# Kernel optimization log

Measured on AMD Instinct MI355X. Metric: run time of the kernel, lower is better.

Reference implementation:

```python
import jax, jax.numpy as jnp
import numpy as np

HEADS = 8
EMBED = 768
FFN = 4 * EMBED
LN_EPS = 1e-5


def _layernorm(x, g, b):
    m = jnp.mean(x, axis=-1, keepdims=True)
    v = jnp.var(x, axis=-1, keepdims=True)
    return (x - m) * jax.lax.rsqrt(v + LN_EPS) * g + b


def _attention(xn, ctx, Wq, Wkv, Wo, bo, mask):
    # xn: [B, N, C], ctx: [B, M, C], mask: [B, 1, N, M] bool (True = keep)
    B, N, C = xn.shape
    d = C // HEADS
    q = (xn @ Wq).reshape(B, N, HEADS, d).transpose(0, 2, 1, 3)          # b h i d
    k, v = jnp.split(ctx @ Wkv, 2, axis=-1)
    k = k.reshape(B, -1, HEADS, d).transpose(0, 2, 1, 3)                 # b h j d
    v = v.reshape(B, -1, HEADS, d).transpose(0, 2, 1, 3)
    sim = jnp.einsum('bhid,bhjd->bhij', q, k) * (d ** -0.5)
    sim = jnp.where(mask, sim, -jnp.finfo(sim.dtype).max)
    attn = jax.nn.softmax(sim, axis=-1)
    out = jnp.einsum('bhij,bhjd->bhid', attn, v)
    out = out.transpose(0, 2, 1, 3).reshape(B, N, C)
    return out @ Wo + bo


def _block(x, c, effect_lengths, us_rate,
           Wq1, Wkv1, Wo1, bo1, Wq2, Wkv2, Wo2, bo2,
           g1, b1, g2, b2, g4, b4, gc, bc, Wf1, bf1, Wf2, bf2):
    B, L, C = x.shape
    S = c.shape[1]
    el = effect_lengths * us_rate                                        # [B]
    i = jnp.arange(L)
    j_self = jnp.arange(L)
    j_cross = jnp.arange(S)
    # ragged per-sample masks, broadcast over heads: [B, 1, L, L] / [B, 1, L, S]
    mask1 = ((i[None, :, None] < el[:, None, None]) &
             (j_self[None, None, :] < el[:, None, None]))[:, None]
    mask2 = ((i[None, :, None] < el[:, None, None]) &
             (j_cross[None, None, :] < effect_lengths[:, None, None]))[:, None]

    xn = _layernorm(x, g1, b1)
    x = x + _attention(xn, xn, Wq1, Wkv1, Wo1, bo1, mask1)
    xn = _layernorm(x, g2, b2)
    cn = _layernorm(c, gc, bc)
    x = x + _attention(xn, cn, Wq2, Wkv2, Wo2, bo2, mask2)
    xn = _layernorm(x, g4, b4)
    x = x + (jax.nn.gelu(xn @ Wf1 + bf1, approximate=False) @ Wf2 + bf2)
    return x


def setup_inputs() -> dict:
    key = jax.random.key(0)
    ks = jax.random.split(key, 20)
    B, S, US = 8, 512, 2
    L = S * US
    s = 0.02
    inp = {
        'x': jax.random.normal(ks[0], (B, L, EMBED), jnp.float32),
        'c': jax.random.normal(ks[1], (B, S, EMBED), jnp.float32),
        'effect_lengths': jax.random.randint(ks[2], (B,), 1, S + 1),
        'us_rate': US,
        'Wq1': jax.random.normal(ks[3], (EMBED, EMBED), jnp.float32) * s,
        'Wkv1': jax.random.normal(ks[4], (EMBED, 2 * EMBED), jnp.float32) * s,
        'Wo1': jax.random.normal(ks[5], (EMBED, EMBED), jnp.float32) * s,
        'bo1': jnp.zeros((EMBED,), jnp.float32),
        'Wq2': jax.random.normal(ks[6], (EMBED, EMBED), jnp.float32) * s,
        'Wkv2': jax.random.normal(ks[7], (EMBED, 2 * EMBED), jnp.float32) * s,
        'Wo2': jax.random.normal(ks[8], (EMBED, EMBED), jnp.float32) * s,
        'bo2': jnp.zeros((EMBED,), jnp.float32),
        'g1': jnp.ones((EMBED,), jnp.float32), 'b1': jnp.zeros((EMBED,), jnp.float32),
        'g2': jnp.ones((EMBED,), jnp.float32), 'b2': jnp.zeros((EMBED,), jnp.float32),
        'g4': jnp.ones((EMBED,), jnp.float32), 'b4': jnp.zeros((EMBED,), jnp.float32),
        'gc': jnp.ones((EMBED,), jnp.float32), 'bc': jnp.zeros((EMBED,), jnp.float32),
        'Wf1': jax.random.normal(ks[9], (EMBED, FFN), jnp.float32) * s,
        'bf1': jnp.zeros((FFN,), jnp.float32),
        'Wf2': jax.random.normal(ks[10], (FFN, EMBED), jnp.float32) * s,
        'bf2': jnp.zeros((EMBED,), jnp.float32),
    }
    return inp


def reference(x, c, effect_lengths, us_rate,
              Wq1, Wkv1, Wo1, bo1, Wq2, Wkv2, Wo2, bo2,
              g1, b1, g2, b2, g4, b4, gc, bc, Wf1, bf1, Wf2, bf2):
    return _block(x, c, effect_lengths, us_rate,
                  Wq1, Wkv1, Wo1, bo1, Wq2, Wkv2, Wo2, bo2,
                  g1, b1, g2, b2, g4, b4, gc, bc, Wf1, bf1, Wf2, bf2)
```

## Files before the change

kernel.cpp:

```cpp
#include <hip/hip_runtime.h>
#include <math.h>

#define EMBED 768
#define HEADS 8
#define HDIM  96
#define NEG_MASK (-1.0e30f)

typedef unsigned short u16;
typedef unsigned int   u32;

typedef __attribute__((ext_vector_type(4))) float f32x4;
typedef __attribute__((ext_vector_type(8))) short short8;

__device__ __forceinline__ float bf2f(u16 u) {
    return __uint_as_float(((u32)u) << 16);
}
__device__ __forceinline__ u16 f2bf(float f) {
    u32 x = __float_as_uint(f);
    u32 r = (x + 0x7fffu + ((x >> 16) & 1u)) >> 16;
    return (u16)r;
}
__device__ __forceinline__ void unpack2(u32 w, float& lo, float& hi) {
    lo = __uint_as_float(w << 16);
    hi = __uint_as_float(w & 0xffff0000u);
}
__device__ __forceinline__ float wget(const void* p, size_t i, int wf) {
    return wf ? ((const float*)p)[i] : bf2f(((const u16*)p)[i]);
}
__device__ __forceinline__ int bswz(int r, int g) {
    return ((g ^ (r & 3) ^ ((r >> 2) & 3) ^ ((r >> 4) & 3)) << 3);
}

__global__ __launch_bounds__(64) void detect_kernel(const u16* __restrict__ x,
                                                    const int* __restrict__ el,
                                                    const int* __restrict__ usp,
                                                    int* __restrict__ blk) {
    int lane = threadIdx.x;
    int cnt = 0;
    for (int i = lane; i < 4096; i += 64) {
        u32 e = (x[i] >> 7) & 0xFFu;
        if (e >= 0xC0u) cnt++;
    }
#pragma unroll
    for (int off = 32; off > 0; off >>= 1) cnt += __shfl_xor(cnt, off, 64);
    if (lane == 0) {
        blk[0] = (cnt > 32) ? 1 : 0;
        bool i64 = (el[1] == 0) && (el[3] == 0) && (el[5] == 0) && (el[7] == 0);
        for (int b = 0; b < 8; b++) blk[1 + b] = i64 ? el[2 * b] : el[b];
        blk[9] = usp[0];
    }
}

__global__ void wire_to_f32(const void* __restrict__ in, size_t ioff,
                            float* __restrict__ out, int n,
                            const int* __restrict__ blk) {
    int i = blockIdx.x * blockDim.x + threadIdx.x;
    int wf = blk[0];
    if (i < n) out[i] = wget(in, ioff + (size_t)i, wf);
}
__global__ void wire_copy(const void* __restrict__ in, void* __restrict__ out,
                          int n, const int* __restrict__ blk) {
    int i = blockIdx.x * blockDim.x + threadIdx.x;
    int wf = blk[0];
    if (i < n) {
        if (wf) ((float*)out)[i] = ((const float*)in)[i];
        else    ((u16*)out)[i]   = ((const u16*)in)[i];
    }
}
__global__ void f32_to_out(const float* __restrict__ in, void* __restrict__ out,
                           size_t ooff, int n, const int* __restrict__ blk) {
    int i = blockIdx.x * blockDim.x + threadIdx.x;
    int wf = blk[0];
    if (i < n) {
        if (wf) ((float*)out)[ooff + i] = in[i];
        else    ((u16*)out)[ooff + i]   = f2bf(in[i]);
    }
}

__global__ __launch_bounds__(256) void wtrans_kernel(const void* __restrict__ W, size_t woff,
                                                     int ldw, int K,
                                                     u16* __restrict__ WT,
                                                     const int* __restrict__ blk) {
    __shared__ u16 T[64][65];
    int wf = blk[0];
    int n0 = blockIdx.x * 64, k0 = blockIdx.y * 64;
    int tid = threadIdx.x;
    int tr = tid >> 4, tc4 = (tid & 15) * 4;
#pragma unroll
    for (int i = 0; i < 4; i++) {
        int k = tr + i * 16;
        if (wf) {
            const float* src = (const float*)W + woff + (size_t)(k0 + k) * ldw + n0 + tc4;
            float4 f = *(const float4*)src;
            T[tc4 + 0][k] = f2bf(f.x); T[tc4 + 1][k] = f2bf(f.y);
            T[tc4 + 2][k] = f2bf(f.z); T[tc4 + 3][k] = f2bf(f.w);
        } else {
            const u16* src = (const u16*)W + woff + (size_t)(k0 + k) * ldw + n0 + tc4;
            uint2 u = *(const uint2*)src;
            T[tc4 + 0][k] = (u16)(u.x & 0xffffu); T[tc4 + 1][k] = (u16)(u.x >> 16);
            T[tc4 + 2][k] = (u16)(u.y & 0xffffu); T[tc4 + 3][k] = (u16)(u.y >> 16);
        }
    }
    __syncthreads();
#pragma unroll
    for (int i = 0; i < 4; i++) {
        int n = tr + i * 16;
        u32 w0 = (u32)T[n][tc4 + 0] | ((u32)T[n][tc4 + 1] << 16);
        u32 w1 = (u32)T[n][tc4 + 2] | ((u32)T[n][tc4 + 3] << 16);
        *(uint2*)(WT + (size_t)(n0 + n) * K + k0 + tc4) = make_uint2(w0, w1);
    }
}

__global__ __launch_bounds__(256) void ln_kernel(const void* __restrict__ in,
                                                 size_t ioff, int sel,
                                                 const void* __restrict__ g,
                                                 const void* __restrict__ b,
                                                 u16* __restrict__ out,
                                                 const int* __restrict__ blk) {
    int wf = blk[0];
    int row = blockIdx.x, tid = threadIdx.x;
    size_t base = ioff + (size_t)row * EMBED;
    float v[3];
#pragma unroll
    for (int e = 0; e < 3; e++) {
        size_t idx = base + tid + e * 256;
        v[e] = (sel == 0) ? ((const float*)in)[idx] : wget(in, idx, wf);
    }
    float s = v[0] + v[1] + v[2];
    float q = v[0] * v[0] + v[1] * v[1] + v[2] * v[2];
#pragma unroll
    for (int off = 32; off > 0; off >>= 1) {
        s += __shfl_xor(s, off, 64);
        q += __shfl_xor(q, off, 64);
    }
    __shared__ float sb[8];
    int wid = tid >> 6, lane = tid & 63;
    if (lane == 0) { sb[wid] = s; sb[4 + wid] = q; }
    __syncthreads();
    if (tid == 0) {
        sb[0] = sb[0] + sb[1] + sb[2] + sb[3];
        sb[4] = sb[4] + sb[5] + sb[6] + sb[7];
    }
    __syncthreads();
    float mean = sb[0] * (1.0f / EMBED);
    float var  = sb[4] * (1.0f / EMBED) - mean * mean;
    float rs   = rsqrtf(var + 1e-5f);
    size_t obase = (size_t)row * EMBED;
#pragma unroll
    for (int e = 0; e < 3; e++) {
        int col = tid + e * 256;
        out[obase + col] = f2bf((v[e] - mean) * rs * wget(g, col, wf) + wget(b, col, wf));
    }
}

__global__ __launch_bounds__(256) void gemm_kernel(const u16* __restrict__ A,
                                                   const void* __restrict__ W,
                                                   size_t woff, int ldw,
                                                   const void* __restrict__ bias, int boff,
                                                   void* __restrict__ Cv, size_t coff,
                                                   int M, int N, int K, int flags,
                                                   int tcmode, const int* __restrict__ blk) {
    __shared__ float As[16][64];
    __shared__ float Bs[16][64];
    int wf = blk[0];
    int tid = threadIdx.x;
    int tx = tid & 15, ty = tid >> 4;
    int row0 = blockIdx.y * 64, col0 = blockIdx.x * 64;
    float acc[4][4] = {};
    int ar = tid >> 2, ac4 = tid & 3;
    int br = tid >> 4, bc4 = tid & 15;

    for (int kb = 0; kb < K; kb += 16) {
        {
            uint2 u = *(const uint2*)(A + (size_t)(row0 + ar) * K + kb + ac4 * 4);
            float a0, a1, a2, a3;
            unpack2(u.x, a0, a1); unpack2(u.y, a2, a3);
            As[ac4 * 4 + 0][ar] = a0; As[ac4 * 4 + 1][ar] = a1;
            As[ac4 * 4 + 2][ar] = a2; As[ac4 * 4 + 3][ar] = a3;
        }
        {
            size_t off = woff + (size_t)(kb + br) * ldw + col0 + bc4 * 4;
            if (wf) {
                float4 u = *(const float4*)((const float*)W + off);
                Bs[br][bc4 * 4 + 0] = u.x; Bs[br][bc4 * 4 + 1] = u.y;
                Bs[br][bc4 * 4 + 2] = u.z; Bs[br][bc4 * 4 + 3] = u.w;
            } else {
                uint2 u = *(const uint2*)((const u16*)W + off);
                float b0, b1, b2, b3;
                unpack2(u.x, b0, b1); unpack2(u.y, b2, b3);
                Bs[br][bc4 * 4 + 0] = b0; Bs[br][bc4 * 4 + 1] = b1;
                Bs[br][bc4 * 4 + 2] = b2; Bs[br][bc4 * 4 + 3] = b3;
            }
        }
        __syncthreads();
#pragma unroll
        for (int kk = 0; kk < 16; kk++) {
            float4 a = *(const float4*)&As[kk][ty * 4];
            float4 b = *(const float4*)&Bs[kk][tx * 4];
            float av[4] = {a.x, a.y, a.z, a.w};
            float bv[4] = {b.x, b.y, b.z, b.w};
#pragma unroll
            for (int i = 0; i < 4; i++)
#pragma unroll
                for (int j = 0; j < 4; j++)
                    acc[i][j] += av[i] * bv[j];
        }
        __syncthreads();
    }

#pragma unroll
    for (int i = 0; i < 4; i++) {
        int m = row0 + ty * 4 + i;
#pragma unroll
        for (int j = 0; j < 4; j++) {
            int n = col0 + tx * 4 + j;
            float v = acc[i][j];
            if (flags & 1) v += wget(bias, boff + n, wf);
            if (flags & 2) v = 0.5f * v * (1.0f + erff(v * 0.70710678118654752f));
            size_t idx = coff + (size_t)m * N + n;
            if (tcmode == 0) {
                ((float*)Cv)[idx] += v;
            } else if (tcmode == 1) {
                ((u16*)Cv)[idx] = f2bf(v);
            } else {
                if (wf) ((float*)Cv)[idx] += v;
                else { u16* p = (u16*)Cv; p[idx] = f2bf(v + bf2f(p[idx])); }
            }
        }
    }
}

__global__ __launch_bounds__(256) void gemm_mfma(const u16* __restrict__ A,
                                                 const void* __restrict__ W,
                                                 size_t woff, int ldw,
                                                 const void* __restrict__ bias, int boff,
                                                 void* __restrict__ Cv, size_t coff,
                                                 int M, int N, int K, int flags,
                                                 int tcmode, const int* __restrict__ blk) {
    __shared__ __align__(16) u16 As[128 * 32];
    __shared__ __align__(16) u16 Bs[128 * 32];
    int wf = blk[0];
    int tid = threadIdx.x;
    int wave = tid >> 6, lane = tid & 63;
    int x = lane & 15, g = lane >> 4;
    int wm = wave >> 1, wn = wave & 1;
    int row0 = blockIdx.y * 128, col0 = blockIdx.x * 128;

    int ar  = tid >> 1, ah = tid & 1;
    int bk  = tid >> 3, bn0 = (tid & 7) * 16;

    f32x4 acc[4][4];
#pragma unroll
    for (int i = 0; i < 4; i++)
#pragma unroll
        for (int j = 0; j < 4; j++) acc[i][j] = (f32x4){0.f, 0.f, 0.f, 0.f};

    for (int kb = 0; kb < K; kb += 32) {
        {
            const u16* asrc = A + (size_t)(row0 + ar) * K + kb + ah * 16;
            uint4 a0 = *(const uint4*)asrc;
            uint4 a1 = *(const uint4*)(asrc + 8);
            *(uint4*)&As[ar * 32 + bswz(ar, ah * 2 + 0)] = a0;
            *(uint4*)&As[ar * 32 + bswz(ar, ah * 2 + 1)] = a1;
        }
        {
            u16 bv[16];
            if (wf) {
                const float* wsrc = (const float*)W + woff + (size_t)(kb + bk) * ldw + col0 + bn0;
#pragma unroll
                for (int i = 0; i < 16; i += 4) {
                    float4 f = *(const float4*)(wsrc + i);
                    bv[i + 0] = f2bf(f.x); bv[i + 1] = f2bf(f.y);
                    bv[i + 2] = f2bf(f.z); bv[i + 3] = f2bf(f.w);
                }
            } else {
                const u16* wsrc = (const u16*)W + woff + (size_t)(kb + bk) * ldw + col0 + bn0;
                ((uint4*)bv)[0] = *(const uint4*)wsrc;
                ((uint4*)bv)[1] = *(const uint4*)(wsrc + 8);
            }
            int kg = bk >> 3, kl = bk & 7;
#pragma unroll
            for (int i = 0; i < 16; i++)
                Bs[(bn0 + i) * 32 + bswz(bn0 + i, kg) + kl] = bv[i];
        }
        __syncthreads();

        short8 af[4], bf[4];
#pragma unroll
        for (int mt = 0; mt < 4; mt++) {
            int r = wm * 64 + mt * 16 + x;
            af[mt] = *(const short8*)&As[r * 32 + bswz(r, g)];
        }
#pragma unroll
        for (int nt = 0; nt < 4; nt++) {
            int n = wn * 64 + nt * 16 + x;
            bf[nt] = *(const short8*)&Bs[n * 32 + bswz(n, g)];
        }
#pragma unroll
        for (int mt = 0; mt < 4; mt++)
#pragma unroll
            for (int nt = 0; nt < 4; nt++)
                acc[mt][nt] = __builtin_amdgcn_mfma_f32_16x16x32_bf16(af[mt], bf[nt], acc[mt][nt], 0, 0, 0);
        __syncthreads();
    }

#pragma unroll
    for (int mt = 0; mt < 4; mt++) {
#pragma unroll
        for (int nt = 0; nt < 4; nt++) {
#pragma unroll
            for (int r = 0; r < 4; r++) {
                int m = row0 + wm * 64 + mt * 16 + g * 4 + r;
                int n = col0 + wn * 64 + nt * 16 + x;
                float v = acc[mt][nt][r];
                if (flags & 1) v += wget(bias, boff + n, wf);
                if (flags & 2) v = 0.5f * v * (1.0f + erff(v * 0.70710678118654752f));
                size_t idx = coff + (size_t)m * N + n;
                if (tcmode == 0) {
                    ((float*)Cv)[idx] += v;
                } else if (tcmode == 1) {
                    ((u16*)Cv)[idx] = f2bf(v);
                } else {
                    if (wf) ((float*)Cv)[idx] += v;
                    else { u16* p = (u16*)Cv; p[idx] = f2bf(v + bf2f(p[idx])); }
                }
            }
        }
    }
}

__global__ __launch_bounds__(256) void gemm_mfma_t(const u16* __restrict__ A,
                                                   const u16* __restrict__ BT,
                                                   const void* __restrict__ bias, int boff,
                                                   void* __restrict__ Cv, size_t coff,
                                                   int M, int N, int K, int flags,
                                                   int tcmode, const int* __restrict__ blk) {
    __shared__ __align__(16) u16 As[2][128 * 32];
    __shared__ __align__(16) u16 Bs[2][128 * 32];
    int wf = blk[0];
    int tid = threadIdx.x;
    int wave = tid >> 6, lane = tid & 63;
    int x = lane & 15, g = lane >> 4;
    int wm = wave >> 1, wn = wave & 1;
    int row0 = blockIdx.y * 128, col0 = blockIdx.x * 128;

    int sr = tid >> 1;
    int sg = (tid & 1) * 2;
    const u16* aptr = A  + (size_t)(row0 + sr) * K + sg * 8;
    const u16* bptr = BT + (size_t)(col0 + sr) * K + sg * 8;
    int wo0 = sr * 32 + bswz(sr, sg);
    int wo1 = sr * 32 + bswz(sr, sg + 1);

    int ra[4], rb[4];
#pragma unroll
    for (int t = 0; t < 4; t++) {
        int r = wm * 64 + t * 16 + x;
        int n = wn * 64 + t * 16 + x;
        ra[t] = r * 32 + bswz(r, g);
        rb[t] = n * 32 + bswz(n, g);
    }

    f32x4 acc[4][4];
#pragma unroll
    for (int i = 0; i < 4; i++)
#pragma unroll
        for (int j = 0; j < 4; j++) acc[i][j] = (f32x4){0.f, 0.f, 0.f, 0.f};

    {
        uint4 a0 = *(const uint4*)aptr, a1 = *(const uint4*)(aptr + 8);
        uint4 b0 = *(const uint4*)bptr, b1 = *(const uint4*)(bptr + 8);
        *(uint4*)&As[0][wo0] = a0; *(uint4*)&As[0][wo1] = a1;
        *(uint4*)&Bs[0][wo0] = b0; *(uint4*)&Bs[0][wo1] = b1;
    }
    __syncthreads();

    int nsteps = K >> 5;
    int cur = 0;
    for (int s = 0; s < nsteps - 1; ++s) {
        aptr += 32; bptr += 32;
        uint4 pa0 = *(const uint4*)aptr, pa1 = *(const uint4*)(aptr + 8);
        uint4 pb0 = *(const uint4*)bptr, pb1 = *(const uint4*)(bptr + 8);

        short8 af[4], bfr[4];
#pragma unroll
        for (int mt = 0; mt < 4; mt++) af[mt] = *(const short8*)&As[cur][ra[mt]];
#pragma unroll
        for (int nt = 0; nt < 4; nt++) bfr[nt] = *(const short8*)&Bs[cur][rb[nt]];
#pragma unroll
        for (int mt = 0; mt < 4; mt++)
#pragma unroll
            for (int nt = 0; nt < 4; nt++)
                acc[mt][nt] = __builtin_amdgcn_mfma_f32_16x16x32_bf16(af[mt], bfr[nt], acc[mt][nt], 0, 0, 0);

        *(uint4*)&As[cur ^ 1][wo0] = pa0; *(uint4*)&As[cur ^ 1][wo1] = pa1;
        *(uint4*)&Bs[cur ^ 1][wo0] = pb0; *(uint4*)&Bs[cur ^ 1][wo1] = pb1;
        __syncthreads();
        cur ^= 1;
    }
    {
        short8 af[4], bfr[4];
#pragma unroll
        for (int mt = 0; mt < 4; mt++) af[mt] = *(const short8*)&As[cur][ra[mt]];
#pragma unroll
        for (int nt = 0; nt < 4; nt++) bfr[nt] = *(const short8*)&Bs[cur][rb[nt]];
#pragma unroll
        for (int mt = 0; mt < 4; mt++)
#pragma unroll
            for (int nt = 0; nt < 4; nt++)
                acc[mt][nt] = __builtin_amdgcn_mfma_f32_16x16x32_bf16(af[mt], bfr[nt], acc[mt][nt], 0, 0, 0);
    }

#pragma unroll
    for (int mt = 0; mt < 4; mt++) {
#pragma unroll
        for (int nt = 0; nt < 4; nt++) {
#pragma unroll
            for (int r = 0; r < 4; r++) {
                int m = row0 + wm * 64 + mt * 16 + g * 4 + r;
                int n = col0 + wn * 64 + nt * 16 + x;
                float v = acc[mt][nt][r];
                if (flags & 1) v += wget(bias, boff + n, wf);
                if (flags & 2) v = 0.5f * v * (1.0f + erff(v * 0.70710678118654752f));
                size_t idx = coff + (size_t)m * N + n;
                if (tcmode == 0) {
                    ((float*)Cv)[idx] += v;
                } else if (tcmode == 1) {
                    ((u16*)Cv)[idx] = f2bf(v);
                } else {
                    if (wf) ((float*)Cv)[idx] += v;
                    else { u16* p = (u16*)Cv; p[idx] = f2bf(v + bf2f(p[idx])); }
                }
            }
        }
    }
}

__global__ __launch_bounds__(256) void attn_kernel(const u16* __restrict__ Q,
                                                   const u16* __restrict__ K,
                                                   const u16* __restrict__ V,
                                                   u16* __restrict__ AO,
                                                   int ldq, int ldk, int ldv, int ldo,
                                                   size_t qss, size_t kss, size_t oss,
                                                   const int* __restrict__ blk,
                                                   int bfix, int Lk, int is_self) {
    int bz   = (bfix < 0) ? blockIdx.z : 0;
    int bidx = (bfix < 0) ? blockIdx.z : bfix;
    const u16* Qp = Q + (size_t)bz * qss;
    const u16* Kp = K + (size_t)bz * kss;
    const u16* Vp = V + (size_t)bz * kss;
    u16* AOp = AO + (size_t)bz * oss;

    int hoff = blockIdx.y * HDIM;
    int i0 = blockIdx.x * 64;
    int tid = threadIdx.x;
    int wave = tid >> 6, lane = tid & 63;
    int x = lane & 15, g = lane >> 4;

    int elb = blk[1 + bidx];
    int el_q = elb * blk[9];
    int el_k = is_self ? el_q : elb;

    __shared__ __align__(16) u16 Ks[64 * 96];
    __shared__ __align__(16) u16 Vs[96 * 64];
    __shared__ __align__(16) u16 Ps[4][16 * 72];

    short8 qf[3];
    {
        const u16* qrow = Qp + (size_t)(i0 + wave * 16 + x) * ldq + hoff;
#pragma unroll
        for (int kc = 0; kc < 3; kc++)
            qf[kc] = *(const short8*)(qrow + kc * 32 + g * 8);
    }

    const f32x4 zero4 = {0.f, 0.f, 0.f, 0.f};
    f32x4 o[6];
#pragma unroll
    for (int dt = 0; dt < 6; dt++) o[dt] = zero4;
    float m[4], l[4];
#pragma unroll
    for (int r = 0; r < 4; r++) { m[r] = NEG_MASK; l[r] = 0.f; }

    bool qok[4];
#pragma unroll
    for (int r = 0; r < 4; r++) qok[r] = (i0 + wave * 16 + g * 4 + r) < el_q;

    const float scale = 0.10206207261596576f;
    u16* pw = &Ps[wave][0];

    for (int kt0 = 0; kt0 < Lk; kt0 += 64) {
#pragma unroll
        for (int t = 0; t < 3; t++) {
            int idx = tid + t * 256;
            int j = idx / 12, c = idx % 12;
            *(uint4*)&Ks[j * 96 + c * 8] =
                *(const uint4*)(Kp + (size_t)(kt0 + j) * ldk + hoff + c * 8);
            uint4 vu = *(const uint4*)(Vp + (size_t)(kt0 + j) * ldv + hoff + c * 8);
            u16 vv[8] = {(u16)(vu.x & 0xffffu), (u16)(vu.x >> 16),
                         (u16)(vu.y & 0xffffu), (u16)(vu.y >> 16),
                         (u16)(vu.z & 0xffffu), (u16)(vu.z >> 16),
                         (u16)(vu.w & 0xffffu), (u16)(vu.w >> 16)};
            int jb = j >> 3, jl = j & 7;
#pragma unroll
            for (int ii = 0; ii < 8; ii++) {
                int d = c * 8 + ii;
                int sb = jb ^ (d & 7) ^ ((d >> 3) & 7);
                Vs[d * 64 + sb * 8 + jl] = vv[ii];
            }
        }
        __syncthreads();

        f32x4 st[4];
#pragma unroll
        for (int t = 0; t < 4; t++) {
            f32x4 acc = zero4;
#pragma unroll
            for (int kc = 0; kc < 3; kc++) {
                short8 kf = *(const short8*)&Ks[(t * 16 + x) * 96 + kc * 32 + g * 8];
                acc = __builtin_amdgcn_mfma_f32_16x16x32_bf16(qf[kc], kf, acc, 0, 0, 0);
            }
            st[t] = acc;
        }

#pragma unroll
        for (int t = 0; t < 4; t++) {
            bool kv_ok = (kt0 + t * 16 + x) < el_k;
#pragma unroll
            for (int r = 0; r < 4; r++)
                st[t][r] = (kv_ok && qok[r]) ? st[t][r] * scale : NEG_MASK;
        }

        float al[4];
#pragma unroll
        for (int r = 0; r < 4; r++) {
            float rm = fmaxf(fmaxf(st[0][r], st[1][r]), fmaxf(st[2][r], st[3][r]));
            rm = fmaxf(rm, __shfl_xor(rm, 1, 64));
            rm = fmaxf(rm, __shfl_xor(rm, 2, 64));
            rm = fmaxf(rm, __shfl_xor(rm, 4, 64));
            rm = fmaxf(rm, __shfl_xor(rm, 8, 64));
            float mn = fmaxf(m[r], rm);
            al[r] = __expf(m[r] - mn);
            m[r] = mn;
            l[r] *= al[r];
        }
#pragma unroll
        for (int dt = 0; dt < 6; dt++)
#pragma unroll
            for (int r = 0; r < 4; r++) o[dt][r] *= al[r];

#pragma unroll
        for (int t = 0; t < 4; t++)
#pragma unroll
            for (int r = 0; r < 4; r++) {
                float p = __expf(st[t][r] - m[r]);
                l[r] += p;
                pw[(g * 4 + r) * 72 + t * 16 + x] = f2bf(p);
            }

#pragma unroll
        for (int kc = 0; kc < 2; kc++) {
            short8 pf = *(const short8*)&pw[x * 72 + kc * 32 + g * 8];
#pragma unroll
            for (int dt = 0; dt < 6; dt++) {
                int d = dt * 16 + x;
                int sb = (kc * 4 + g) ^ (d & 7) ^ ((d >> 3) & 7);
                short8 vf = *(const short8*)&Vs[d * 64 + sb * 8];
                o[dt] = __builtin_amdgcn_mfma_f32_16x16x32_bf16(pf, vf, o[dt], 0, 0, 0);
            }
        }
        __syncthreads();
    }

    float inv[4];
#pragma unroll
    for (int r = 0; r < 4; r++) {
        float lr = l[r];
        lr += __shfl_xor(lr, 1, 64);
        lr += __shfl_xor(lr, 2, 64);
        lr += __shfl_xor(lr, 4, 64);
        lr += __shfl_xor(lr, 8, 64);
        inv[r] = 1.0f / lr;
    }
#pragma unroll
    for (int dt = 0; dt < 6; dt++)
#pragma unroll
        for (int r = 0; r < 4; r++) {
            size_t ob = (size_t)(i0 + wave * 16 + g * 4 + r) * ldo + hoff + dt * 16 + x;
            AOp[ob] = f2bf(o[dt][r] * inv[r]);
        }
}

extern "C" void kernel_launch(void* const* d_in, const int* in_sizes, int n_in,
                              void* d_out, int out_size, void* d_ws, size_t ws_size,
                              hipStream_t stream) {
    const void* x    = d_in[0];
    const void* c    = d_in[1];
    const int* el    = (const int*)d_in[2];
    const int* us    = (const int*)d_in[3];
    const void* Wq1  = d_in[4];
    const void* Wkv1 = d_in[5];
    const void* Wo1  = d_in[6];
    const void* bo1  = d_in[7];
    const void* Wq2  = d_in[8];
    const void* Wkv2 = d_in[9];
    const void* Wo2  = d_in[10];
    const void* bo2  = d_in[11];
    const void* g1 = d_in[12]; const void* b1 = d_in[13];
    const void* g2 = d_in[14]; const void* b2 = d_in[15];
    const void* g4 = d_in[16]; const void* b4 = d_in[17];
    const void* gc = d_in[18]; const void* bc = d_in[19];
    const void* Wf1 = d_in[20]; const void* bf1 = d_in[21];
    const void* Wf2 = d_in[22]; const void* bf2 = d_in[23];

    const int B = 8, S = 512, L = 1024, C = EMBED;
    const int NX = B * L * C;
    const size_t RL = (size_t)L * C;
    const size_t RS = (size_t)S * C;

    char* ws = (char*)d_ws;
    int*  blk = (int*)ws;
    dim3 blkd(256);

    bool tierA = ws_size >= (size_t)88080448;
    bool tierB = !tierA && ws_size >= (size_t)33030208;

    detect_kernel<<<1, 64, 0, stream>>>((const u16*)x, el, us, blk);

    if (tierA) {
        float* X  = (float*)(ws + 64);
        u16*   XN = (u16*)(ws + 25165888);
        u16*   WT = (u16*)(ws + 37748800);
        char*  P  = ws + 47185984;
        u16* Qb   = (u16*)P;
        u16* KVb  = (u16*)(P + 12582912);
        u16* CNb  = (u16*)P;
        u16* KV2b = (u16*)(P + 6291456);
        u16* Q2b  = (u16*)(P + 18874368);
        u16* Hh   = (u16*)P;
        const size_t WTq = 0, WTkv = 589824, WTo = 1769472;
        const size_t WTf1 = 0, WTf2 = 2359296;

        wire_to_f32<<<(NX + 255) / 256, blkd, 0, stream>>>(x, 0, X, NX, blk);

        wtrans_kernel<<<dim3(12, 12), blkd, 0, stream>>>(Wq1, 0, C, C, WT + WTq, blk);
        wtrans_kernel<<<dim3(24, 12), blkd, 0, stream>>>(Wkv1, 0, 2 * C, C, WT + WTkv, blk);
        wtrans_kernel<<<dim3(12, 12), blkd, 0, stream>>>(Wo1, 0, C, C, WT + WTo, blk);

        ln_kernel<<<B * L, blkd, 0, stream>>>(X, 0, 0, g1, b1, XN, blk);
        gemm_mfma_t<<<dim3(6, 64), blkd, 0, stream>>>(XN, WT + WTq, nullptr, 0, Qb, 0, B * L, C, C, 0, 1, blk);
        gemm_mfma_t<<<dim3(12, 64), blkd, 0, stream>>>(XN, WT + WTkv, nullptr, 0, KVb, 0, B * L, 2 * C, C, 0, 1, blk);
        attn_kernel<<<dim3(16, 8, 8), blkd, 0, stream>>>(Qb, KVb, KVb + C, Qb, C, 2 * C, 2 * C, C,
                                                         RL, (size_t)L * 2 * C, RL, blk, -1, L, 1);
        gemm_mfma_t<<<dim3(6, 64), blkd, 0, stream>>>(Qb, WT + WTo, bo1, 0, X, 0, B * L, C, C, 1, 0, blk);

        wtrans_kernel<<<dim3(12, 12), blkd, 0, stream>>>(Wq2, 0, C, C, WT + WTq, blk);
        wtrans_kernel<<<dim3(24, 12), blkd, 0, stream>>>(Wkv2, 0, 2 * C, C, WT + WTkv, blk);
        wtrans_kernel<<<dim3(12, 12), blkd, 0, stream>>>(Wo2, 0, C, C, WT + WTo, blk);

        ln_kernel<<<B * L, blkd, 0, stream>>>(X, 0, 0, g2, b2, XN, blk);
        ln_kernel<<<B * S, blkd, 0, stream>>>(c, 0, 2, gc, bc, CNb, blk);
        gemm_mfma_t<<<dim3(12, 32), blkd, 0, stream>>>(CNb, WT + WTkv, nullptr, 0, KV2b, 0, B * S, 2 * C, C, 0, 1, blk);
        gemm_mfma_t<<<dim3(6, 64), blkd, 0, stream>>>(XN, WT + WTq, nullptr, 0, Q2b, 0, B * L, C, C, 0, 1, blk);
        attn_kernel<<<dim3(16, 8, 8), blkd, 0, stream>>>(Q2b, KV2b, KV2b + C, Q2b, C, 2 * C, 2 * C, C,
                                                         RL, (size_t)S * 2 * C, RL, blk, -1, S, 0);
        gemm_mfma_t<<<dim3(6, 64), blkd, 0, stream>>>(Q2b, WT + WTo, bo2, 0, X, 0, B * L, C, C, 1, 0, blk);

        wtrans_kernel<<<dim3(48, 12), blkd, 0, stream>>>(Wf1, 0, 4 * C, C, WT + WTf1, blk);
        wtrans_kernel<<<dim3(12, 48), blkd, 0, stream>>>(Wf2, 0, C, 4 * C, WT + WTf2, blk);

        ln_kernel<<<B * L, blkd, 0, stream>>>(X, 0, 0, g4, b4, XN, blk);
        for (int h = 0; h < 2; h++) {
            size_t ro = (size_t)h * 4096 * C;
            gemm_mfma_t<<<dim3(24, 32), blkd, 0, stream>>>(XN + ro, WT + WTf1, bf1, 0, Hh, 0, 4096, 4 * C, C, 1 | 2, 1, blk);
            gemm_mfma_t<<<dim3(6, 32), blkd, 0, stream>>>(Hh, WT + WTf2, bf2, 0, X, ro, 4096, C, 4 * C, 1, 0, blk);
        }

        f32_to_out<<<(NX + 255) / 256, blkd, 0, stream>>>(X, d_out, 0, NX, blk);
    } else if (tierB) {
        float* X  = (float*)(ws + 64);
        u16*   XN = (u16*)(ws + 64 + 25165824);
        char*  P  = ws + 64 + 25165824 + 1572864;
        u16* Qb   = (u16*)P;
        u16* KVb  = (u16*)(P + 1572864);
        u16* AOb  = (u16*)(P + 4718592);
        u16* CNb  = (u16*)P;
        u16* KV2b = (u16*)(P + 786432);
        u16* Q2b  = (u16*)(P + 2359296);
        u16* AO2b = (u16*)(P + 3932160);
        u16* Hb   = (u16*)P;

        wire_to_f32<<<(NX + 255) / 256, blkd, 0, stream>>>(x, 0, X, NX, blk);

        for (int b = 0; b < B; b++) {
            size_t ro = (size_t)b * RL;
            ln_kernel<<<L, blkd, 0, stream>>>(X, ro, 0, g1, b1, XN, blk);
            gemm_mfma<<<dim3(6, 8), blkd, 0, stream>>>(XN, Wq1, 0, C, nullptr, 0, Qb, 0, L, C, C, 0, 1, blk);
            gemm_mfma<<<dim3(12, 8), blkd, 0, stream>>>(XN, Wkv1, 0, 2 * C, nullptr, 0, KVb, 0, L, 2 * C, C, 0, 1, blk);
            attn_kernel<<<dim3(16, 8), blkd, 0, stream>>>(Qb, KVb, KVb + C, AOb, C, 2 * C, 2 * C, C, 0, 0, 0, blk, b, L, 1);
            gemm_mfma<<<dim3(6, 8), blkd, 0, stream>>>(AOb, Wo1, 0, C, bo1, 0, X, ro, L, C, C, 1, 0, blk);

            ln_kernel<<<L, blkd, 0, stream>>>(X, ro, 0, g2, b2, XN, blk);
            ln_kernel<<<S, blkd, 0, stream>>>(c, (size_t)b * RS, 2, gc, bc, CNb, blk);
            gemm_mfma<<<dim3(12, 4), blkd, 0, stream>>>(CNb, Wkv2, 0, 2 * C, nullptr, 0, KV2b, 0, S, 2 * C, C, 0, 1, blk);
            gemm_mfma<<<dim3(6, 8), blkd, 0, stream>>>(XN, Wq2, 0, C, nullptr, 0, Q2b, 0, L, C, C, 0, 1, blk);
            attn_kernel<<<dim3(16, 8), blkd, 0, stream>>>(Q2b, KV2b, KV2b + C, AO2b, C, 2 * C, 2 * C, C, 0, 0, 0, blk, b, S, 0);
            gemm_mfma<<<dim3(6, 8), blkd, 0, stream>>>(AO2b, Wo2, 0, C, bo2, 0, X, ro, L, C, C, 1, 0, blk);

            ln_kernel<<<L, blkd, 0, stream>>>(X, ro, 0, g4, b4, XN, blk);
            gemm_mfma<<<dim3(24, 8), blkd, 0, stream>>>(XN, Wf1, 0, 4 * C, bf1, 0, Hb, 0, L, 4 * C, C, 1 | 2, 1, blk);
            gemm_mfma<<<dim3(6, 8), blkd, 0, stream>>>(Hb, Wf2, 0, C, bf2, 0, X, ro, L, C, 4 * C, 1, 0, blk);
        }
        f32_to_out<<<(NX + 255) / 256, blkd, 0, stream>>>(X, d_out, 0, NX, blk);
    } else {
        u16*  XN  = (u16*)(ws + 64);
        u16*  CNb = (u16*)(ws + 64 + 1572864);
        char* P2  = ws + 64 + 1572864 + 786432;
        u16* Qp  = (u16*)P2;
        u16* Kp  = (u16*)(P2 + 393216);
        u16* Vp  = (u16*)(P2 + 786432);
        u16* AOp = (u16*)(P2 + 1179648);
        u16* Hc  = (u16*)P2;

        wire_copy<<<(NX + 255) / 256, blkd, 0, stream>>>(x, d_out, NX, blk);

        for (int b = 0; b < B; b++) {
            size_t ro = (size_t)b * RL;

            ln_kernel<<<L, blkd, 0, stream>>>(d_out, ro, 2, g1, b1, XN, blk);
            for (int p = 0; p < 4; p++) {
                int h = 2 * p;
                gemm_kernel<<<dim3(3, 16), blkd, 0, stream>>>(XN, Wq1, (size_t)h * 96, C, nullptr, 0, Qp, 0, L, 192, C, 0, 1, blk);
                gemm_kernel<<<dim3(3, 16), blkd, 0, stream>>>(XN, Wkv1, (size_t)h * 96, 2 * C, nullptr, 0, Kp, 0, L, 192, C, 0, 1, blk);
                gemm_kernel<<<dim3(3, 16), blkd, 0, stream>>>(XN, Wkv1, (size_t)(C + h * 96), 2 * C, nullptr, 0, Vp, 0, L, 192, C, 0, 1, blk);
                attn_kernel<<<dim3(16, 2), blkd, 0, stream>>>(Qp, Kp, Vp, AOp, 192, 192, 192, 192, 0, 0, 0, blk, b, L, 1);
                gemm_kernel<<<dim3(12, 16), blkd, 0, stream>>>(AOp, Wo1, (size_t)h * 96 * C, C, bo1, 0, d_out, ro, L, C, 192, (p == 0) ? 1 : 0, 3, blk);
            }
            ln_kernel<<<L, blkd, 0, stream>>>(d_out, ro, 2, g2, b2, XN, blk);
            ln_kernel<<<S, blkd, 0, stream>>>(c, (size_t)b * RS, 2, gc, bc, CNb, blk);
            for (int p = 0; p < 4; p++) {
                int h = 2 * p;
                gemm_kernel<<<dim3(3, 16), blkd, 0, stream>>>(XN, Wq2, (size_t)h * 96, C, nullptr, 0, Qp, 0, L, 192, C, 0, 1, blk);
                gemm_kernel<<<dim3(3, 8), blkd, 0, stream>>>(CNb, Wkv2, (size_t)h * 96, 2 * C, nullptr, 0, Kp, 0, S, 192, C, 0, 1, blk);
                gemm_kernel<<<dim3(3, 8), blkd, 0, stream>>>(CNb, Wkv2, (size_t)(C + h * 96), 2 * C, nullptr, 0, Vp, 0, S, 192, C, 0, 1, blk);
                attn_kernel<<<dim3(16, 2), blkd, 0, stream>>>(Qp, Kp, Vp, AOp, 192, 192, 192, 192, 0, 0, 0, blk, b, S, 0);
                gemm_kernel<<<dim3(12, 16), blkd, 0, stream>>>(AOp, Wo2, (size_t)h * 96 * C, C, bo2, 0, d_out, ro, L, C, 192, (p == 0) ? 1 : 0, 3, blk);
            }
            ln_kernel<<<L, blkd, 0, stream>>>(d_out, ro, 2, g4, b4, XN, blk);
            for (int ch = 0; ch < 4; ch++) {
                gemm_kernel<<<dim3(12, 16), blkd, 0, stream>>>(XN, Wf1, (size_t)ch * C, 4 * C, bf1, ch * C, Hc, 0, L, C, C, 1 | 2, 1, blk);
                gemm_kernel<<<dim3(12, 16), blkd, 0, stream>>>(Hc, Wf2, (size_t)ch * C * C, C, bf2, 0, d_out, ro, L, C, C, (ch == 0) ? 1 : 0, 3, blk);
            }
        }
    }
}
```

Baseline: 895.4 us.

## Add split-K with atomic accumulation and two-stage register prefetch in GEMM

The GEMM kernel now splits the K dimension across gridDim.z. Each slice accumulates its partial result into the fp32 residual buffer with atomicAdd, and only the first slice adds the bias. The main loop is unrolled by two and keeps two register sets of global prefetches, so loads for step s+2 are issued while step s computes. Split-K of 2 is enabled for the output-projection and FFN2 GEMMs, which otherwise launch only 384 or 192 blocks. The intent is better CU occupancy and more latency hiding, at the cost of atomic traffic, more register pressure and a non-deterministic summation order.

```diff
diff --git a/kernel.cpp b/kernel.cpp
--- a/kernel.cpp
+++ b/kernel.cpp
@@ -343,11 +343,13 @@
     int x = lane & 15, g = lane >> 4;
     int wm = wave >> 1, wn = wave & 1;
     int row0 = blockIdx.y * 128, col0 = blockIdx.x * 128;
+    int KS = gridDim.z, kz = blockIdx.z;
+    int Kc = K / KS;
 
     int sr = tid >> 1;
     int sg = (tid & 1) * 2;
-    const u16* aptr = A  + (size_t)(row0 + sr) * K + sg * 8;
-    const u16* bptr = BT + (size_t)(col0 + sr) * K + sg * 8;
+    const u16* aptr = A  + (size_t)(row0 + sr) * K + kz * Kc + sg * 8;
+    const u16* bptr = BT + (size_t)(col0 + sr) * K + kz * Kc + sg * 8;
     int wo0 = sr * 32 + bswz(sr, sg);
     int wo1 = sr * 32 + bswz(sr, sg + 1);
 
@@ -366,50 +368,59 @@
 #pragma unroll
         for (int j = 0; j < 4; j++) acc[i][j] = (f32x4){0.f, 0.f, 0.f, 0.f};
 
+    int nsteps = Kc >> 5;
+
     {
         uint4 a0 = *(const uint4*)aptr, a1 = *(const uint4*)(aptr + 8);
         uint4 b0 = *(const uint4*)bptr, b1 = *(const uint4*)(bptr + 8);
         *(uint4*)&As[0][wo0] = a0; *(uint4*)&As[0][wo1] = a1;
         *(uint4*)&Bs[0][wo0] = b0; *(uint4*)&Bs[0][wo1] = b1;
     }
+    uint4 s0a0 = {}, s0a1 = {}, s0b0 = {}, s0b1 = {};
+    uint4 s1a0 = {}, s1a1 = {}, s1b0 = {}, s1b1 = {};
+    if (nsteps > 1) {
+        aptr += 32; bptr += 32;
+        s1a0 = *(const uint4*)aptr; s1a1 = *(const uint4*)(aptr + 8);
+        s1b0 = *(const uint4*)bptr; s1b1 = *(const uint4*)(bptr + 8);
+    }
     __syncthreads();
 
-    int nsteps = K >> 5;
-    int cur = 0;
-    for (int s = 0; s < nsteps - 1; ++s) {
-        aptr += 32; bptr += 32;
-        uint4 pa0 = *(const uint4*)aptr, pa1 = *(const uint4*)(aptr + 8);
-        uint4 pb0 = *(const uint4*)bptr, pb1 = *(const uint4*)(bptr + 8);
-
-        short8 af[4], bfr[4];
-#pragma unroll
-        for (int mt = 0; mt < 4; mt++) af[mt] = *(const short8*)&As[cur][ra[mt]];
-#pragma unroll
-        for (int nt = 0; nt < 4; nt++) bfr[nt] = *(const short8*)&Bs[cur][rb[nt]];
-#pragma unroll
-        for (int mt = 0; mt < 4; mt++)
-#pragma unroll
-            for (int nt = 0; nt < 4; nt++)
-                acc[mt][nt] = __builtin_amdgcn_mfma_f32_16x16x32_bf16(af[mt], bfr[nt], acc[mt][nt], 0, 0, 0);
-
-        *(uint4*)&As[cur ^ 1][wo0] = pa0; *(uint4*)&As[cur ^ 1][wo1] = pa1;
-        *(uint4*)&Bs[cur ^ 1][wo0] = pb0; *(uint4*)&Bs[cur ^ 1][wo1] = pb1;
-        __syncthreads();
-        cur ^= 1;
-    }
-    {
-        short8 af[4], bfr[4];
-#pragma unroll
-        for (int mt = 0; mt < 4; mt++) af[mt] = *(const short8*)&As[cur][ra[mt]];
-#pragma unroll
-        for (int nt = 0; nt < 4; nt++) bfr[nt] = *(const short8*)&Bs[cur][rb[nt]];
-#pragma unroll
-        for (int mt = 0; mt < 4; mt++)
-#pragma unroll
-            for (int nt = 0; nt < 4; nt++)
-                acc[mt][nt] = __builtin_amdgcn_mfma_f32_16x16x32_bf16(af[mt], bfr[nt], acc[mt][nt], 0, 0, 0);
-    }
-
+#define GSTEP(S, LA0, LA1, LB0, LB1, WA0, WA1, WB0, WB1)                          \
+    {                                                                             \
+        if ((S) + 2 < nsteps) {                                                   \
+            aptr += 32; bptr += 32;                                               \
+            LA0 = *(const uint4*)aptr; LA1 = *(const uint4*)(aptr + 8);           \
+            LB0 = *(const uint4*)bptr; LB1 = *(const uint4*)(bptr + 8);           \
+        }                                                                         \
+        short8 af[4], bfr[4];                                                     \
+        _Pragma("unroll")                                                         \
+        for (int mt = 0; mt < 4; mt++)                                            \
+            af[mt] = *(const short8*)&As[(S) & 1][ra[mt]];                        \
+        _Pragma("unroll")                                                         \
+        for (int nt = 0; nt < 4; nt++)                                            \
+            bfr[nt] = *(const short8*)&Bs[(S) & 1][rb[nt]];                       \
+        _Pragma("unroll")                                                         \
+        for (int mt = 0; mt < 4; mt++)                                            \
+            _Pragma("unroll")                                                     \
+            for (int nt = 0; nt < 4; nt++)                                        \
+                acc[mt][nt] = __builtin_amdgcn_mfma_f32_16x16x32_bf16(            \
+                    af[mt], bfr[nt], acc[mt][nt], 0, 0, 0);                       \
+        if ((S) + 1 < nsteps) {                                                   \
+            int nb = (((S) & 1) ^ 1);                                             \
+            *(uint4*)&As[nb][wo0] = WA0; *(uint4*)&As[nb][wo1] = WA1;             \
+            *(uint4*)&Bs[nb][wo0] = WB0; *(uint4*)&Bs[nb][wo1] = WB1;             \
+            __syncthreads();                                                      \
+        }                                                                         \
+    }
+
+    for (int s = 0; s < nsteps; s += 2) {
+        GSTEP(s, s0a0, s0a1, s0b0, s0b1, s1a0, s1a1, s1b0, s1b1);
+        if (s + 1 < nsteps)
+            GSTEP(s + 1, s1a0, s1a1, s1b0, s1b1, s0a0, s0a1, s0b0, s0b1);
+    }
+#undef GSTEP
+
+    bool kz0 = (kz == 0);
 #pragma unroll
     for (int mt = 0; mt < 4; mt++) {
 #pragma unroll
@@ -419,11 +430,12 @@
                 int m = row0 + wm * 64 + mt * 16 + g * 4 + r;
                 int n = col0 + wn * 64 + nt * 16 + x;
                 float v = acc[mt][nt][r];
-                if (flags & 1) v += wget(bias, boff + n, wf);
+                if ((flags & 1) && kz0) v += wget(bias, boff + n, wf);
                 if (flags & 2) v = 0.5f * v * (1.0f + erff(v * 0.70710678118654752f));
                 size_t idx = coff + (size_t)m * N + n;
                 if (tcmode == 0) {
-                    ((float*)Cv)[idx] += v;
+                    if (KS > 1) atomicAdd(&((float*)Cv)[idx], v);
+                    else        ((float*)Cv)[idx] += v;
                 } else if (tcmode == 1) {
                     ((u16*)Cv)[idx] = f2bf(v);
                 } else {
@@ -646,11 +658,11 @@
         wtrans_kernel<<<dim3(12, 12), blkd, 0, stream>>>(Wo1, 0, C, C, WT + WTo, blk);
 
         ln_kernel<<<B * L, blkd, 0, stream>>>(X, 0, 0, g1, b1, XN, blk);
-        gemm_mfma_t<<<dim3(6, 64), blkd, 0, stream>>>(XN, WT + WTq, nullptr, 0, Qb, 0, B * L, C, C, 0, 1, blk);
-        gemm_mfma_t<<<dim3(12, 64), blkd, 0, stream>>>(XN, WT + WTkv, nullptr, 0, KVb, 0, B * L, 2 * C, C, 0, 1, blk);
+        gemm_mfma_t<<<dim3(6, 64, 1), blkd, 0, stream>>>(XN, WT + WTq, nullptr, 0, Qb, 0, B * L, C, C, 0, 1, blk);
+        gemm_mfma_t<<<dim3(12, 64, 1), blkd, 0, stream>>>(XN, WT + WTkv, nullptr, 0, KVb, 0, B * L, 2 * C, C, 0, 1, blk);
         attn_kernel<<<dim3(16, 8, 8), blkd, 0, stream>>>(Qb, KVb, KVb + C, Qb, C, 2 * C, 2 * C, C,
                                                          RL, (size_t)L * 2 * C, RL, blk, -1, L, 1);
-        gemm_mfma_t<<<dim3(6, 64), blkd, 0, stream>>>(Qb, WT + WTo, bo1, 0, X, 0, B * L, C, C, 1, 0, blk);
+        gemm_mfma_t<<<dim3(6, 64, 2), blkd, 0, stream>>>(Qb, WT + WTo, bo1, 0, X, 0, B * L, C, C, 1, 0, blk);
 
         wtrans_kernel<<<dim3(12, 12), blkd, 0, stream>>>(Wq2, 0, C, C, WT + WTq, blk);
         wtrans_kernel<<<dim3(24, 12), blkd, 0, stream>>>(Wkv2, 0, 2 * C, C, WT + WTkv, blk);
@@ -658,11 +670,11 @@
 
         ln_kernel<<<B * L, blkd, 0, stream>>>(X, 0, 0, g2, b2, XN, blk);
         ln_kernel<<<B * S, blkd, 0, stream>>>(c, 0, 2, gc, bc, CNb, blk);
-        gemm_mfma_t<<<dim3(12, 32), blkd, 0, stream>>>(CNb, WT + WTkv, nullptr, 0, KV2b, 0, B * S, 2 * C, C, 0, 1, blk);
-        gemm_mfma_t<<<dim3(6, 64), blkd, 0, stream>>>(XN, WT + WTq, nullptr, 0, Q2b, 0, B * L, C, C, 0, 1, blk);
+        gemm_mfma_t<<<dim3(12, 32, 1), blkd, 0, stream>>>(CNb, WT + WTkv, nullptr, 0, KV2b, 0, B * S, 2 * C, C, 0, 1, blk);
+        gemm_mfma_t<<<dim3(6, 64, 1), blkd, 0, stream>>>(XN, WT + WTq, nullptr, 0, Q2b, 0, B * L, C, C, 0, 1, blk);
         attn_kernel<<<dim3(16, 8, 8), blkd, 0, stream>>>(Q2b, KV2b, KV2b + C, Q2b, C, 2 * C, 2 * C, C,
                                                          RL, (size_t)S * 2 * C, RL, blk, -1, S, 0);
-        gemm_mfma_t<<<dim3(6, 64), blkd, 0, stream>>>(Q2b, WT + WTo, bo2, 0, X, 0, B * L, C, C, 1, 0, blk);
+        gemm_mfma_t<<<dim3(6, 64, 2), blkd, 0, stream>>>(Q2b, WT + WTo, bo2, 0, X, 0, B * L, C, C, 1, 0, blk);
 
         wtrans_kernel<<<dim3(48, 12), blkd, 0, stream>>>(Wf1, 0, 4 * C, C, WT + WTf1, blk);
         wtrans_kernel<<<dim3(12, 48), blkd, 0, stream>>>(Wf2, 0, C, 4 * C, WT + WTf2, blk);
@@ -670,8 +682,8 @@
         ln_kernel<<<B * L, blkd, 0, stream>>>(X, 0, 0, g4, b4, XN, blk);
         for (int h = 0; h < 2; h++) {
             size_t ro = (size_t)h * 4096 * C;
-            gemm_mfma_t<<<dim3(24, 32), blkd, 0, stream>>>(XN + ro, WT + WTf1, bf1, 0, Hh, 0, 4096, 4 * C, C, 1 | 2, 1, blk);
-            gemm_mfma_t<<<dim3(6, 32), blkd, 0, stream>>>(Hh, WT + WTf2, bf2, 0, X, ro, 4096, C, 4 * C, 1, 0, blk);
+            gemm_mfma_t<<<dim3(24, 32, 1), blkd, 0, stream>>>(XN + ro, WT + WTf1, bf1, 0, Hh, 0, 4096, 4 * C, C, 1 | 2, 1, blk);
+            gemm_mfma_t<<<dim3(6, 32, 2), blkd, 0, stream>>>(Hh, WT + WTf2, bf2, 0, X, ro, 4096, C, 4 * C, 1, 0, blk);
         }
 
         f32_to_out<<<(NX + 255) / 256, blkd, 0, stream>>>(X, d_out, 0, NX, blk);
```

Measured after the change: 924.0 us. 3.2% more time.
